# Performance work log

Measured on AMD Instinct MI355X. Metric: run time of the kernel, lower is better.

Reference implementation:

```python
import jax, jax.numpy as jnp
import numpy as np

B, S, D = 2, 2048, 1024
H, HD = 16, 64
MLP = 4096
EPS = 1e-5


def layer_norm(x, g, b):
    mu = jnp.mean(x, axis=-1, keepdims=True)
    var = jnp.mean(jnp.square(x - mu), axis=-1, keepdims=True)
    return (x - mu) * jax.lax.rsqrt(var + EPS) * g + b


def setup_inputs() -> dict:
    key = jax.random.key(0)
    ks = jax.random.split(key, 12)
    s = 0.02
    return {
        "x": jax.random.normal(ks[0], (B, S, D), jnp.float32),
        "ln1_g": jnp.ones((D,), jnp.float32),
        "ln1_b": jnp.zeros((D,), jnp.float32),
        "Wq": jax.random.normal(ks[1], (D, H * HD), jnp.float32) * s,
        "Wk": jax.random.normal(ks[2], (D, H * HD), jnp.float32) * s,
        "Wv": jax.random.normal(ks[3], (D, H * HD), jnp.float32) * s,
        "Wo": jax.random.normal(ks[4], (H * HD, D), jnp.float32) * s,
        "ln2_g": jnp.ones((D,), jnp.float32),
        "ln2_b": jnp.zeros((D,), jnp.float32),
        "fc1_w": jax.random.normal(ks[5], (D, MLP), jnp.float32) * s,
        "fc1_b": jnp.zeros((MLP,), jnp.float32),
        "fc2_w": jax.random.normal(ks[6], (MLP, D), jnp.float32) * s,
        "fc2_b": jnp.zeros((D,), jnp.float32),
    }


def reference(x, ln1_g, ln1_b, Wq, Wk, Wv, Wo, ln2_g, ln2_b, fc1_w, fc1_b, fc2_w, fc2_b):
    b, s, d = x.shape
    scale = 1.0 / np.sqrt(HD)
    h = layer_norm(x, ln1_g, ln1_b)
    # project and split heads: [b, H, s, HD]
    q = (h @ Wq).reshape(b, s, H, HD).transpose(0, 2, 1, 3)
    k = (h @ Wk).reshape(b, s, H, HD).transpose(0, 2, 1, 3)
    v = (h @ Wv).reshape(b, s, H, HD).transpose(0, 2, 1, 3)
    scores = jnp.einsum('bhqd,bhkd->bhqk', q, k) * scale
    causal = jnp.where(jnp.tril(jnp.ones((s, s), bool)), 0.0, -jnp.inf).astype(x.dtype)
    scores = scores + causal[None, None]
    attn_weights = jax.nn.softmax(scores, axis=-1)
    attn_out = jnp.einsum('bhqk,bhkd->bhqd', attn_weights, v)
    attn_out = attn_out.transpose(0, 2, 1, 3).reshape(b, s, H * HD) @ Wo
    x = x + attn_out
    h2 = layer_norm(x, ln2_g, ln2_b)
    mlp = jax.nn.gelu(h2 @ fc1_w + fc1_b, approximate=True) @ fc2_w + fc2_b
    x = x + mlp
    return (x, attn_weights)
```

## Files before the change

### kernel.cpp

```cpp
#include <hip/hip_runtime.h>
#include <cmath>

typedef __bf16 bf16;
typedef __bf16 bf16x8 __attribute__((ext_vector_type(8)));
typedef float f32x4 __attribute__((ext_vector_type(4)));

#define B_ 2
#define S_ 2048
#define D_ 1024
#define H_ 16
#define HD_ 64
#define MLP_ 4096
#define XOUT_ ((size_t)B_ * S_ * D_)

__device__ __forceinline__ void gll16(const void* g, void* l) {
  __builtin_amdgcn_global_load_lds((const __attribute__((address_space(1))) void*)g,
                                   (__attribute__((address_space(3))) void*)l, 16, 0, 0);
}

__device__ __forceinline__ f32x4 mfma16(bf16x8 a, bf16x8 b, f32x4 c) {
  return __builtin_amdgcn_mfma_f32_16x16x32_bf16(a, b, c, 0, 0, 0);
}

__device__ __forceinline__ float bfu2f(unsigned short u) {
  return __uint_as_float(((unsigned int)u) << 16);
}
__device__ __forceinline__ unsigned short f2bu(float v) {
  union { bf16 b; unsigned short u; } c; c.b = (bf16)v; return c.u;
}
__device__ __forceinline__ float ld_sc(const void* p, size_t i, int f32) {
  return f32 ? ((const float*)p)[i] : bfu2f(((const unsigned short*)p)[i]);
}

__global__ __launch_bounds__(64) void detect_k(const unsigned short* __restrict__ x,
                                               int* __restrict__ flag) {
  int tid = threadIdx.x;
  int cnt = 0;
  for (int i = tid; i < 512; i += 64) {
    int e = (x[i] >> 7) & 0xFF;
    if (e >= 0xBF) cnt++;
  }
  #pragma unroll
  for (int d = 1; d < 64; d <<= 1) cnt += __shfl_xor(cnt, d);
  if (tid == 0) flag[0] = (cnt > 8) ? 1 : 0;
}

__global__ __launch_bounds__(256) void transpose_ad(const void* __restrict__ in,
                                                    unsigned short* __restrict__ out,
                                                    int R, int C,
                                                    const int* __restrict__ flagp) {
  __shared__ unsigned short t[64][68];
  const int f32 = flagp[0];
  const int tid = threadIdx.x;
  const int c0 = blockIdx.x * 64, r0 = blockIdx.y * 64;
  for (int i = tid * 4; i < 4096; i += 1024) {
    int rr = i >> 6, cc = i & 63;
    size_t off = (size_t)(r0 + rr) * C + c0 + cc;
    if (f32) {
      float4 f = *(const float4*)((const float*)in + off);
      t[rr][cc + 0] = f2bu(f.x); t[rr][cc + 1] = f2bu(f.y);
      t[rr][cc + 2] = f2bu(f.z); t[rr][cc + 3] = f2bu(f.w);
    } else {
      *(ushort4*)&t[rr][cc] = *(const ushort4*)((const unsigned short*)in + off);
    }
  }
  __syncthreads();
  for (int i = tid * 4; i < 4096; i += 1024) {
    int orr = i & 63, oc = i >> 6;
    ushort4 v;
    v.x = t[orr + 0][oc]; v.y = t[orr + 1][oc];
    v.z = t[orr + 2][oc]; v.w = t[orr + 3][oc];
    *(ushort4*)(out + (size_t)(c0 + oc) * R + r0 + orr) = v;
  }
}

__global__ __launch_bounds__(256) void vtrans_k(const unsigned short* __restrict__ qkv,
                                                unsigned short* __restrict__ vT) {
  __shared__ unsigned short t[64][68];
  const int tid = threadIdx.x;
  const int s0 = blockIdx.x * 64, h = blockIdx.y, b = blockIdx.z;
  for (int i = tid * 4; i < 4096; i += 1024) {
    int si = i >> 6, hd = i & 63;
    *(ushort4*)&t[si][hd] =
        *(const ushort4*)(qkv + (size_t)(b * S_ + s0 + si) * 3072 + 2048 + h * 64 + hd);
  }
  __syncthreads();
  for (int i = tid * 4; i < 4096; i += 1024) {
    int ss = i & 63, hd = i >> 6;
    ushort4 v;
    v.x = t[ss + 0][hd]; v.y = t[ss + 1][hd];
    v.z = t[ss + 2][hd]; v.w = t[ss + 3][hd];
    *(ushort4*)(vT + ((size_t)(b * H_ + h) * 64 + hd) * S_ + s0 + ss) = v;
  }
}

__global__ __launch_bounds__(256) void ln_k(const void* __restrict__ xv,
                                            const void* __restrict__ g,
                                            const void* __restrict__ bvec,
                                            bf16* __restrict__ out,
                                            const int* __restrict__ flagp,
                                            int force_xf32) {
  const int f32 = flagp[0];
  const int xf32 = force_xf32 ? 1 : f32;
  const int row = blockIdx.x, tid = threadIdx.x;
  float v[4];
  if (xf32) {
    float4 f = *(const float4*)((const float*)xv + (size_t)row * 1024 + tid * 4);
    v[0] = f.x; v[1] = f.y; v[2] = f.z; v[3] = f.w;
  } else {
    ushort4 u = *(const ushort4*)((const unsigned short*)xv + (size_t)row * 1024 + tid * 4);
    v[0] = bfu2f(u.x); v[1] = bfu2f(u.y); v[2] = bfu2f(u.z); v[3] = bfu2f(u.w);
  }
  float s = 0.f, q = 0.f;
  #pragma unroll
  for (int i = 0; i < 4; i++) { s += v[i]; q += v[i] * v[i]; }
  #pragma unroll
  for (int d = 1; d < 64; d <<= 1) { s += __shfl_xor(s, d); q += __shfl_xor(q, d); }
  __shared__ float red[8];
  if ((tid & 63) == 0) { red[(tid >> 6) * 2] = s; red[(tid >> 6) * 2 + 1] = q; }
  __syncthreads();
  s = red[0] + red[2] + red[4] + red[6];
  q = red[1] + red[3] + red[5] + red[7];
  const float mean = s * (1.0f / 1024.0f);
  const float var = q * (1.0f / 1024.0f) - mean * mean;
  const float rs = rsqrtf(var + 1e-5f);
  unsigned short ov[4];
  #pragma unroll
  for (int i = 0; i < 4; i++) {
    float gg = ld_sc(g, tid * 4 + i, f32);
    float bb = ld_sc(bvec, tid * 4 + i, f32);
    ov[i] = f2bu((v[i] - mean) * rs * gg + bb);
  }
  ushort4 o4; o4.x = ov[0]; o4.y = ov[1]; o4.z = ov[2]; o4.w = ov[3];
  *(ushort4*)((unsigned short*)out + (size_t)row * 1024 + tid * 4) = o4;
}

template <int MODE>
__global__ __launch_bounds__(256) void gemm_bt(const bf16* __restrict__ A,
                                               const bf16* __restrict__ BT,
                                               int N, int K,
                                               const void* __restrict__ bias,
                                               const void* __restrict__ resb,
                                               const float* __restrict__ resf,
                                               bf16* __restrict__ outb,
                                               float* __restrict__ outf,
                                               const int* __restrict__ flagp) {
  __shared__ __align__(16) bf16 sA[128 * 64];
  __shared__ __align__(16) bf16 sB[128 * 64];
  const int f32 = flagp[0];
  const int tid = threadIdx.x;
  const int lane = tid & 63;
  const int wave = tid >> 6;
  const int wm = wave >> 1, wn = wave & 1;
  const int m0 = blockIdx.y * 128, n0 = blockIdx.x * 128;
  const int cn = lane & 15, rl = lane >> 4;
  const int r0 = tid >> 3, c16 = tid & 7;

  f32x4 zero = {0.f, 0.f, 0.f, 0.f};
  f32x4 acc[4][4];
  #pragma unroll
  for (int i = 0; i < 4; i++)
    #pragma unroll
    for (int j = 0; j < 4; j++) acc[i][j] = zero;

  for (int k0 = 0; k0 < K; k0 += 64) {
    __syncthreads();
    #pragma unroll
    for (int i = 0; i < 4; i++) {
      int row = r0 + i * 32;
      gll16(A + (size_t)(m0 + row) * K + k0 + c16 * 8, &sA[row * 64 + c16 * 8]);
      gll16(BT + (size_t)(n0 + row) * K + k0 + c16 * 8, &sB[row * 64 + c16 * 8]);
    }
    __syncthreads();
    #pragma unroll
    for (int kk = 0; kk < 64; kk += 32) {
      bf16x8 af[4], bfr[4];
      #pragma unroll
      for (int t = 0; t < 4; t++) {
        af[t] = *(const bf16x8*)&sA[(wm * 64 + t * 16 + cn) * 64 + kk + rl * 8];
        bfr[t] = *(const bf16x8*)&sB[(wn * 64 + t * 16 + cn) * 64 + kk + rl * 8];
      }
      #pragma unroll
      for (int mt = 0; mt < 4; mt++)
        #pragma unroll
        for (int nt = 0; nt < 4; nt++)
          acc[mt][nt] = mfma16(af[mt], bfr[nt], acc[mt][nt]);
    }
  }

  #pragma unroll
  for (int mt = 0; mt < 4; mt++) {
    #pragma unroll
    for (int nt = 0; nt < 4; nt++) {
      #pragma unroll
      for (int j = 0; j < 4; j++) {
        const int row = m0 + wm * 64 + mt * 16 + rl * 4 + j;
        const int col = n0 + wn * 64 + nt * 16 + cn;
        const size_t idx = (size_t)row * N + col;
        float v = acc[mt][nt][j];
        if (MODE == 0) {
          outb[idx] = (bf16)v;
        } else if (MODE == 1) {
          v += ld_sc(bias, col, f32);
          float gl = 0.5f * v * (1.0f + tanhf(0.7978845608028654f * (v + 0.044715f * v * v * v)));
          outb[idx] = (bf16)gl;
        } else if (MODE == 2) {
          outf[idx] = v + ld_sc(resb, idx, f32);
        } else {
          float val = v + ld_sc(bias, col, f32) + resf[idx];
          if (f32) outf[idx] = val; else outb[idx] = (bf16)val;
        }
      }
    }
  }
}

__global__ __launch_bounds__(256) void attn_k(const bf16* __restrict__ qkv,
                                              const bf16* __restrict__ vT,
                                              void* __restrict__ Pv,
                                              bf16* __restrict__ ao,
                                              const int* __restrict__ flagp) {
  __shared__ __align__(16) bf16 sQ[64 * 64];
  __shared__ __align__(16) bf16 sK[64 * 64];
  __shared__ __align__(16) bf16 sV[64 * 64];
  __shared__ __align__(16) bf16 sP[4][16 * 64];
  const int f32o = flagp[0];
  const int tid = threadIdx.x, lane = tid & 63, wave = tid >> 6;
  const int qt = blockIdx.x, h = blockIdx.y, b = blockIdx.z;
  const float scale = 0.125f;
  const float NEG = -1e30f;
  const int cn = lane & 15, rl = lane >> 4;
  const int r0 = tid >> 3, c16 = tid & 7;

  #pragma unroll
  for (int i = 0; i < 2; i++) {
    int row = r0 + i * 32;
    gll16(qkv + (size_t)(b * S_ + qt * 64 + row) * 3072 + h * 64 + c16 * 8,
          &sQ[row * 64 + c16 * 8]);
  }

  float m_i[4], l_i[4];
  #pragma unroll
  for (int j = 0; j < 4; j++) { m_i[j] = NEG; l_i[j] = 0.0f; }

  for (int kt = 0; kt <= qt; kt++) {
    __syncthreads();
    #pragma unroll
    for (int i = 0; i < 2; i++) {
      int row = r0 + i * 32;
      gll16(qkv + (size_t)(b * S_ + kt * 64 + row) * 3072 + 1024 + h * 64 + c16 * 8,
            &sK[row * 64 + c16 * 8]);
    }
    __syncthreads();
    f32x4 s[4];
    f32x4 zero = {0.f, 0.f, 0.f, 0.f};
    #pragma unroll
    for (int nt = 0; nt < 4; nt++) s[nt] = zero;
    #pragma unroll
    for (int kk = 0; kk < 64; kk += 32) {
      bf16x8 a = *(const bf16x8*)&sQ[(wave * 16 + cn) * 64 + kk + rl * 8];
      #pragma unroll
      for (int nt = 0; nt < 4; nt++) {
        bf16x8 bb = *(const bf16x8*)&sK[(nt * 16 + cn) * 64 + kk + rl * 8];
        s[nt] = mfma16(a, bb, s[nt]);
      }
    }
    const int rowg = qt * 64 + wave * 16 + rl * 4;
    const int colg0 = kt * 64 + cn;
    float pm[4] = {NEG, NEG, NEG, NEG};
    #pragma unroll
    for (int nt = 0; nt < 4; nt++)
      #pragma unroll
      for (int j = 0; j < 4; j++) {
        float v = (colg0 + nt * 16 > rowg + j) ? NEG : s[nt][j] * scale;
        s[nt][j] = v;
        pm[j] = fmaxf(pm[j], v);
      }
    #pragma unroll
    for (int j = 0; j < 4; j++) {
      #pragma unroll
      for (int d = 1; d < 16; d <<= 1) pm[j] = fmaxf(pm[j], __shfl_xor(pm[j], d));
      float mn = fmaxf(m_i[j], pm[j]);
      float ps = 0.f;
      #pragma unroll
      for (int nt = 0; nt < 4; nt++) ps += expf(s[nt][j] - mn);
      #pragma unroll
      for (int d = 1; d < 16; d <<= 1) ps += __shfl_xor(ps, d);
      l_i[j] = l_i[j] * expf(m_i[j] - mn) + ps;
      m_i[j] = mn;
    }
  }

  float inv_l[4];
  #pragma unroll
  for (int j = 0; j < 4; j++) inv_l[j] = 1.0f / l_i[j];

  f32x4 o[4];
  {
    f32x4 zero = {0.f, 0.f, 0.f, 0.f};
    #pragma unroll
    for (int nt = 0; nt < 4; nt++) o[nt] = zero;
  }
  for (int kt = 0; kt <= qt; kt++) {
    __syncthreads();
    #pragma unroll
    for (int i = 0; i < 2; i++) {
      int row = r0 + i * 32;
      gll16(qkv + (size_t)(b * S_ + kt * 64 + row) * 3072 + 1024 + h * 64 + c16 * 8,
            &sK[row * 64 + c16 * 8]);
      gll16(vT + ((size_t)(b * H_ + h) * 64 + row) * S_ + kt * 64 + c16 * 8,
            &sV[row * 64 + c16 * 8]);
    }
    __syncthreads();
    f32x4 s[4];
    f32x4 zero = {0.f, 0.f, 0.f, 0.f};
    #pragma unroll
    for (int nt = 0; nt < 4; nt++) s[nt] = zero;
    #pragma unroll
    for (int kk = 0; kk < 64; kk += 32) {
      bf16x8 a = *(const bf16x8*)&sQ[(wave * 16 + cn) * 64 + kk + rl * 8];
      #pragma unroll
      for (int nt = 0; nt < 4; nt++) {
        bf16x8 bb = *(const bf16x8*)&sK[(nt * 16 + cn) * 64 + kk + rl * 8];
        s[nt] = mfma16(a, bb, s[nt]);
      }
    }
    const int rowg = qt * 64 + wave * 16 + rl * 4;
    const int colg0 = kt * 64 + cn;
    #pragma unroll
    for (int nt = 0; nt < 4; nt++)
      #pragma unroll
      for (int j = 0; j < 4; j++) {
        bool masked = (colg0 + nt * 16 > rowg + j);
        float p = masked ? 0.0f : expf(s[nt][j] * scale - m_i[j]) * inv_l[j];
        sP[wave][(rl * 4 + j) * 64 + nt * 16 + cn] = (bf16)p;
      }
    __syncthreads();
    #pragma unroll
    for (int kk = 0; kk < 64; kk += 32) {
      bf16x8 ap = *(const bf16x8*)&sP[wave][cn * 64 + kk + rl * 8];
      #pragma unroll
      for (int nt = 0; nt < 4; nt++) {
        bf16x8 bv = *(const bf16x8*)&sV[(nt * 16 + cn) * 64 + kk + rl * 8];
        o[nt] = mfma16(ap, bv, o[nt]);
      }
    }
    size_t base = XOUT_ + (((size_t)b * H_ + h) * S_ + qt * 64 + wave * 16) * S_ + kt * 64;
    #pragma unroll
    for (int i = 0; i < 2; i++) {
      int idx = lane + i * 64;
      int r = idx >> 3, cc = idx & 7;
      if (f32o) {
        float4 lo, hi;
        const bf16* src = &sP[wave][r * 64 + cc * 8];
        lo.x = (float)src[0]; lo.y = (float)src[1]; lo.z = (float)src[2]; lo.w = (float)src[3];
        hi.x = (float)src[4]; hi.y = (float)src[5]; hi.z = (float)src[6]; hi.w = (float)src[7];
        *(float4*)((float*)Pv + base + (size_t)r * S_ + cc * 8) = lo;
        *(float4*)((float*)Pv + base + (size_t)r * S_ + cc * 8 + 4) = hi;
      } else {
        uint4 val = *(const uint4*)&sP[wave][r * 64 + cc * 8];
        *(uint4*)((bf16*)Pv + base + (size_t)r * S_ + cc * 8) = val;
      }
    }
  }

  {
    const int t0 = qt + 1;
    const int nch = (32 - t0) * 8;
    size_t rowbase = XOUT_ + (((size_t)b * H_ + h) * S_ + qt * 64) * S_;
    uint4 z; z.x = 0; z.y = 0; z.z = 0; z.w = 0;
    for (int idx = tid; idx < 64 * nch; idx += 256) {
      int r = idx / nch, cc = idx % nch;
      size_t off = rowbase + (size_t)r * S_ + t0 * 64 + cc * 8;
      if (f32o) {
        *(uint4*)((float*)Pv + off) = z;
        *(uint4*)((float*)Pv + off + 4) = z;
      } else {
        *(uint4*)((bf16*)Pv + off) = z;
      }
    }
  }

  #pragma unroll
  for (int nt = 0; nt < 4; nt++)
    #pragma unroll
    for (int j = 0; j < 4; j++) {
      int rowg2 = b * S_ + qt * 64 + wave * 16 + rl * 4 + j;
      ao[(size_t)rowg2 * 1024 + h * 64 + nt * 16 + cn] = (bf16)o[nt][j];
    }
}

extern "C" void kernel_launch(void* const* d_in, const int* in_sizes, int n_in,
                              void* d_out, int out_size, void* d_ws, size_t ws_size,
                              hipStream_t stream) {
  (void)in_sizes; (void)n_in; (void)out_size; (void)ws_size;
  const void* x    = d_in[0];
  const void* ln1g = d_in[1];
  const void* ln1b = d_in[2];
  const void* Wq   = d_in[3];
  const void* Wk   = d_in[4];
  const void* Wv   = d_in[5];
  const void* Wo   = d_in[6];
  const void* ln2g = d_in[7];
  const void* ln2b = d_in[8];
  const void* fc1w = d_in[9];
  const void* fc1b = d_in[10];
  const void* fc2w = d_in[11];
  const void* fc2b = d_in[12];

  char* ws = (char*)d_ws;
  bf16* wqkvT = (bf16*)(ws + 0);
  bf16* woT   = (bf16*)(ws + 6291456);
  bf16* fc1T  = (bf16*)(ws + 8388608);
  bf16* fc2T  = (bf16*)(ws + 16777216);
  bf16* h     = (bf16*)(ws + 25165824);
  bf16* qkv   = (bf16*)(ws + 33554432);
  bf16* vT    = (bf16*)(ws + 58720256);
  bf16* m1    = (bf16*)(ws + 33554432);
  bf16* aout  = (bf16*)(ws + 67108864);
  float* x1   = (float*)(ws + 75497472);
  int* flag   = (int*)(ws + 92274688);

  dim3 blk(256);

  detect_k<<<1, 64, 0, stream>>>((const unsigned short*)x, flag);

  transpose_ad<<<dim3(16, 16), blk, 0, stream>>>(Wq, (unsigned short*)wqkvT, 1024, 1024, flag);
  transpose_ad<<<dim3(16, 16), blk, 0, stream>>>(Wk, (unsigned short*)(wqkvT + 1024 * 1024), 1024, 1024, flag);
  transpose_ad<<<dim3(16, 16), blk, 0, stream>>>(Wv, (unsigned short*)(wqkvT + 2 * 1024 * 1024), 1024, 1024, flag);
  transpose_ad<<<dim3(16, 16), blk, 0, stream>>>(Wo, (unsigned short*)woT, 1024, 1024, flag);
  transpose_ad<<<dim3(64, 16), blk, 0, stream>>>(fc1w, (unsigned short*)fc1T, 1024, 4096, flag);
  transpose_ad<<<dim3(16, 64), blk, 0, stream>>>(fc2w, (unsigned short*)fc2T, 4096, 1024, flag);

  ln_k<<<4096, blk, 0, stream>>>(x, ln1g, ln1b, h, flag, 0);

  gemm_bt<0><<<dim3(24, 32), blk, 0, stream>>>(h, wqkvT, 3072, 1024, nullptr, nullptr, nullptr, qkv, nullptr, flag);

  vtrans_k<<<dim3(32, 16, 2), blk, 0, stream>>>((const unsigned short*)qkv, (unsigned short*)vT);

  attn_k<<<dim3(32, 16, 2), blk, 0, stream>>>(qkv, vT, d_out, aout, flag);

  gemm_bt<2><<<dim3(8, 32), blk, 0, stream>>>(aout, woT, 1024, 1024, nullptr, x, nullptr, nullptr, x1, flag);

  ln_k<<<4096, blk, 0, stream>>>(x1, ln2g, ln2b, h, flag, 1);

  gemm_bt<1><<<dim3(32, 32), blk, 0, stream>>>(h, fc1T, 4096, 1024, fc1b, nullptr, nullptr, m1, nullptr, flag);

  gemm_bt<3><<<dim3(8, 32), blk, 0, stream>>>(m1, fc2T, 1024, 4096, fc2b, nullptr, x1, (bf16*)d_out, (float*)d_out, flag);
}
```

Before: 1.155 ms.

## Double-buffer K/V tiles in attention with swizzled LDS and exp2 softmax

The attention kernel now double-buffers K and V tiles in LDS, prefetching the next tile while computing the current one, and waits with explicit vmcnt counts and raw barriers instead of full __syncthreads. LDS layouts are XOR-swizzled to reduce bank conflicts. Q is held in registers, and the causal mask is applied only on the diagonal tile. Query tiles are launched in reverse order so the longest blocks start first. Softmax uses exp2 with a pre-scaled log2e factor, and GELU's tanh is rewritten as a sigmoid via exp2. The explicit vmcnt waits depend on exact counts of outstanding loads and stores, which is fragile if code generation changes.

```diff
diff --git a/kernel.cpp b/kernel.cpp
--- a/kernel.cpp
+++ b/kernel.cpp
@@ -13,6 +13,10 @@
 #define MLP_ 4096
 #define XOUT_ ((size_t)B_ * S_ * D_)
 
+#define SBAR() __builtin_amdgcn_s_barrier()
+#define VMCNT(N) asm volatile("s_waitcnt vmcnt(" #N ")" ::: "memory")
+#define SFENCE() asm volatile("" ::: "memory")
+
 __device__ __forceinline__ void gll16(const void* g, void* l) {
   __builtin_amdgcn_global_load_lds((const __attribute__((address_space(1))) void*)g,
                                    (__attribute__((address_space(3))) void*)l, 16, 0, 0);
@@ -30,6 +34,11 @@
 }
 __device__ __forceinline__ float ld_sc(const void* p, size_t i, int f32) {
   return f32 ? ((const float*)p)[i] : bfu2f(((const unsigned short*)p)[i]);
+}
+
+__device__ __forceinline__ int swz(int row, int col) {
+  int byo = row * 128 + col * 2;
+  return (byo ^ (((byo >> 9) & 3) << 5)) >> 1;
 }
 
 __global__ __launch_bounds__(64) void detect_k(const unsigned short* __restrict__ x,
@@ -202,7 +211,8 @@
           outb[idx] = (bf16)v;
         } else if (MODE == 1) {
           v += ld_sc(bias, col, f32);
-          float gl = 0.5f * v * (1.0f + tanhf(0.7978845608028654f * (v + 0.044715f * v * v * v)));
+          float u = 0.7978845608028654f * (v + 0.044715f * v * v * v);
+          float gl = v / (1.0f + exp2f(-2.8853900817779268f * u));
           outb[idx] = (bf16)gl;
         } else if (MODE == 2) {
           outf[idx] = v + ld_sc(resb, idx, f32);
@@ -220,80 +230,114 @@
                                               void* __restrict__ Pv,
                                               bf16* __restrict__ ao,
                                               const int* __restrict__ flagp) {
-  __shared__ __align__(16) bf16 sQ[64 * 64];
-  __shared__ __align__(16) bf16 sK[64 * 64];
-  __shared__ __align__(16) bf16 sV[64 * 64];
+  __shared__ __align__(16) bf16 sK[2][64 * 64];
+  __shared__ __align__(16) bf16 sV[2][64 * 64];
   __shared__ __align__(16) bf16 sP[4][16 * 64];
   const int f32o = flagp[0];
   const int tid = threadIdx.x, lane = tid & 63, wave = tid >> 6;
-  const int qt = blockIdx.x, h = blockIdx.y, b = blockIdx.z;
-  const float scale = 0.125f;
+  const int qt = (int)(gridDim.x - 1 - blockIdx.x);
+  const int h = blockIdx.y, b = blockIdx.z;
+  const float scale2 = 0.18033688011112042f;
   const float NEG = -1e30f;
   const int cn = lane & 15, rl = lane >> 4;
-  const int r0 = tid >> 3, c16 = tid & 7;
-
+
+  int urow[2], ucol[2], ldst[2];
   #pragma unroll
   for (int i = 0; i < 2; i++) {
-    int row = r0 + i * 32;
-    gll16(qkv + (size_t)(b * S_ + qt * 64 + row) * 3072 + h * 64 + c16 * 8,
-          &sQ[row * 64 + c16 * 8]);
-  }
+    int Lb = tid * 16 + i * 4096;
+    int Ub = Lb ^ (((Lb >> 9) & 3) << 5);
+    urow[i] = Ub >> 7;
+    ucol[i] = (Ub & 127) >> 1;
+    ldst[i] = Lb >> 1;
+  }
+
+  const bf16* kbase = qkv + (size_t)b * S_ * 3072 + 1024 + h * 64;
+  const bf16* vbase = vT + ((size_t)(b * H_ + h) * 64) * S_;
+
+  bf16x8 aq[2];
+  {
+    const bf16* qb = qkv + (size_t)(b * S_ + qt * 64 + wave * 16 + cn) * 3072 + h * 64;
+    aq[0] = *(const bf16x8*)(qb + rl * 8);
+    aq[1] = *(const bf16x8*)(qb + 32 + rl * 8);
+  }
+
+  #pragma unroll
+  for (int i = 0; i < 2; i++)
+    gll16(kbase + (size_t)urow[i] * 3072 + ucol[i], &sK[0][ldst[i]]);
+  VMCNT(0);
+  SBAR();
 
   float m_i[4], l_i[4];
   #pragma unroll
   for (int j = 0; j < 4; j++) { m_i[j] = NEG; l_i[j] = 0.0f; }
 
+  int cur = 0;
   for (int kt = 0; kt <= qt; kt++) {
-    __syncthreads();
-    #pragma unroll
-    for (int i = 0; i < 2; i++) {
-      int row = r0 + i * 32;
-      gll16(qkv + (size_t)(b * S_ + kt * 64 + row) * 3072 + 1024 + h * 64 + c16 * 8,
-            &sK[row * 64 + c16 * 8]);
-    }
-    __syncthreads();
+    if (kt < qt) {
+      #pragma unroll
+      for (int i = 0; i < 2; i++)
+        gll16(kbase + (size_t)((kt + 1) * 64 + urow[i]) * 3072 + ucol[i], &sK[cur ^ 1][ldst[i]]);
+      SFENCE();
+    }
     f32x4 s[4];
     f32x4 zero = {0.f, 0.f, 0.f, 0.f};
     #pragma unroll
     for (int nt = 0; nt < 4; nt++) s[nt] = zero;
     #pragma unroll
-    for (int kk = 0; kk < 64; kk += 32) {
-      bf16x8 a = *(const bf16x8*)&sQ[(wave * 16 + cn) * 64 + kk + rl * 8];
+    for (int kx = 0; kx < 2; kx++)
       #pragma unroll
       for (int nt = 0; nt < 4; nt++) {
-        bf16x8 bb = *(const bf16x8*)&sK[(nt * 16 + cn) * 64 + kk + rl * 8];
-        s[nt] = mfma16(a, bb, s[nt]);
-      }
-    }
-    const int rowg = qt * 64 + wave * 16 + rl * 4;
-    const int colg0 = kt * 64 + cn;
+        bf16x8 bb = *(const bf16x8*)&sK[cur][swz(nt * 16 + cn, kx * 32 + rl * 8)];
+        s[nt] = mfma16(aq[kx], bb, s[nt]);
+      }
     float pm[4] = {NEG, NEG, NEG, NEG};
-    #pragma unroll
-    for (int nt = 0; nt < 4; nt++)
-      #pragma unroll
-      for (int j = 0; j < 4; j++) {
-        float v = (colg0 + nt * 16 > rowg + j) ? NEG : s[nt][j] * scale;
-        s[nt][j] = v;
-        pm[j] = fmaxf(pm[j], v);
-      }
+    if (kt == qt) {
+      #pragma unroll
+      for (int nt = 0; nt < 4; nt++)
+        #pragma unroll
+        for (int j = 0; j < 4; j++) {
+          float v = (nt * 16 + cn > wave * 16 + rl * 4 + j) ? NEG : s[nt][j] * scale2;
+          s[nt][j] = v;
+          pm[j] = fmaxf(pm[j], v);
+        }
+    } else {
+      #pragma unroll
+      for (int nt = 0; nt < 4; nt++)
+        #pragma unroll
+        for (int j = 0; j < 4; j++) {
+          float v = s[nt][j] * scale2;
+          s[nt][j] = v;
+          pm[j] = fmaxf(pm[j], v);
+        }
+    }
     #pragma unroll
     for (int j = 0; j < 4; j++) {
       #pragma unroll
       for (int d = 1; d < 16; d <<= 1) pm[j] = fmaxf(pm[j], __shfl_xor(pm[j], d));
       float mn = fmaxf(m_i[j], pm[j]);
-      float ps = 0.f;
-      #pragma unroll
-      for (int nt = 0; nt < 4; nt++) ps += expf(s[nt][j] - mn);
+      float ps = exp2f(s[0][j] - mn) + exp2f(s[1][j] - mn) +
+                 exp2f(s[2][j] - mn) + exp2f(s[3][j] - mn);
       #pragma unroll
       for (int d = 1; d < 16; d <<= 1) ps += __shfl_xor(ps, d);
-      l_i[j] = l_i[j] * expf(m_i[j] - mn) + ps;
+      l_i[j] = l_i[j] * exp2f(m_i[j] - mn) + ps;
       m_i[j] = mn;
     }
+    if (kt < qt) { VMCNT(0); SBAR(); cur ^= 1; }
   }
 
   float inv_l[4];
   #pragma unroll
   for (int j = 0; j < 4; j++) inv_l[j] = 1.0f / l_i[j];
+
+  SBAR();
+  #pragma unroll
+  for (int i = 0; i < 2; i++) {
+    gll16(kbase + (size_t)urow[i] * 3072 + ucol[i], &sK[0][ldst[i]]);
+    gll16(vbase + (size_t)urow[i] * S_ + ucol[i], &sV[0][ldst[i]]);
+  }
+  VMCNT(0);
+  SBAR();
+  cur = 0;
 
   f32x4 o[4];
   {
@@ -301,66 +345,78 @@
     #pragma unroll
     for (int nt = 0; nt < 4; nt++) o[nt] = zero;
   }
+
   for (int kt = 0; kt <= qt; kt++) {
-    __syncthreads();
-    #pragma unroll
-    for (int i = 0; i < 2; i++) {
-      int row = r0 + i * 32;
-      gll16(qkv + (size_t)(b * S_ + kt * 64 + row) * 3072 + 1024 + h * 64 + c16 * 8,
-            &sK[row * 64 + c16 * 8]);
-      gll16(vT + ((size_t)(b * H_ + h) * 64 + row) * S_ + kt * 64 + c16 * 8,
-            &sV[row * 64 + c16 * 8]);
-    }
-    __syncthreads();
+    if (kt < qt) {
+      #pragma unroll
+      for (int i = 0; i < 2; i++) {
+        gll16(kbase + (size_t)((kt + 1) * 64 + urow[i]) * 3072 + ucol[i], &sK[cur ^ 1][ldst[i]]);
+        gll16(vbase + (size_t)urow[i] * S_ + (kt + 1) * 64 + ucol[i], &sV[cur ^ 1][ldst[i]]);
+      }
+      SFENCE();
+    }
     f32x4 s[4];
     f32x4 zero = {0.f, 0.f, 0.f, 0.f};
     #pragma unroll
     for (int nt = 0; nt < 4; nt++) s[nt] = zero;
     #pragma unroll
-    for (int kk = 0; kk < 64; kk += 32) {
-      bf16x8 a = *(const bf16x8*)&sQ[(wave * 16 + cn) * 64 + kk + rl * 8];
+    for (int kx = 0; kx < 2; kx++)
       #pragma unroll
       for (int nt = 0; nt < 4; nt++) {
-        bf16x8 bb = *(const bf16x8*)&sK[(nt * 16 + cn) * 64 + kk + rl * 8];
-        s[nt] = mfma16(a, bb, s[nt]);
-      }
-    }
-    const int rowg = qt * 64 + wave * 16 + rl * 4;
-    const int colg0 = kt * 64 + cn;
-    #pragma unroll
-    for (int nt = 0; nt < 4; nt++)
-      #pragma unroll
-      for (int j = 0; j < 4; j++) {
-        bool masked = (colg0 + nt * 16 > rowg + j);
-        float p = masked ? 0.0f : expf(s[nt][j] * scale - m_i[j]) * inv_l[j];
-        sP[wave][(rl * 4 + j) * 64 + nt * 16 + cn] = (bf16)p;
-      }
-    __syncthreads();
-    #pragma unroll
-    for (int kk = 0; kk < 64; kk += 32) {
-      bf16x8 ap = *(const bf16x8*)&sP[wave][cn * 64 + kk + rl * 8];
+        bf16x8 bb = *(const bf16x8*)&sK[cur][swz(nt * 16 + cn, kx * 32 + rl * 8)];
+        s[nt] = mfma16(aq[kx], bb, s[nt]);
+      }
+    if (kt == qt) {
+      #pragma unroll
+      for (int nt = 0; nt < 4; nt++)
+        #pragma unroll
+        for (int j = 0; j < 4; j++) {
+          bool masked = (nt * 16 + cn > wave * 16 + rl * 4 + j);
+          float p = masked ? 0.0f : exp2f(s[nt][j] * scale2 - m_i[j]) * inv_l[j];
+          sP[wave][swz(rl * 4 + j, nt * 16 + cn)] = (bf16)p;
+        }
+    } else {
+      #pragma unroll
+      for (int nt = 0; nt < 4; nt++)
+        #pragma unroll
+        for (int j = 0; j < 4; j++) {
+          float p = exp2f(s[nt][j] * scale2 - m_i[j]) * inv_l[j];
+          sP[wave][swz(rl * 4 + j, nt * 16 + cn)] = (bf16)p;
+        }
+    }
+    {
+      size_t base = XOUT_ + (((size_t)b * H_ + h) * S_ + qt * 64 + wave * 16) * S_ + kt * 64;
+      #pragma unroll
+      for (int i = 0; i < 2; i++) {
+        int idx = lane + i * 64;
+        int r = idx >> 3, cc = idx & 7;
+        uint4 val = *(const uint4*)&sP[wave][swz(r, cc * 8)];
+        if (f32o) {
+          float4 lo, hi;
+          lo.x = __uint_as_float(val.x << 16); lo.y = __uint_as_float(val.x & 0xffff0000u);
+          lo.z = __uint_as_float(val.y << 16); lo.w = __uint_as_float(val.y & 0xffff0000u);
+          hi.x = __uint_as_float(val.z << 16); hi.y = __uint_as_float(val.z & 0xffff0000u);
+          hi.z = __uint_as_float(val.w << 16); hi.w = __uint_as_float(val.w & 0xffff0000u);
+          *(float4*)((float*)Pv + base + (size_t)r * S_ + cc * 8) = lo;
+          *(float4*)((float*)Pv + base + (size_t)r * S_ + cc * 8 + 4) = hi;
+        } else {
+          *(uint4*)((bf16*)Pv + base + (size_t)r * S_ + cc * 8) = val;
+        }
+      }
+    }
+    #pragma unroll
+    for (int kx = 0; kx < 2; kx++) {
+      bf16x8 ap = *(const bf16x8*)&sP[wave][swz(cn, kx * 32 + rl * 8)];
       #pragma unroll
       for (int nt = 0; nt < 4; nt++) {
-        bf16x8 bv = *(const bf16x8*)&sV[(nt * 16 + cn) * 64 + kk + rl * 8];
+        bf16x8 bv = *(const bf16x8*)&sV[cur][swz(nt * 16 + cn, kx * 32 + rl * 8)];
         o[nt] = mfma16(ap, bv, o[nt]);
       }
     }
-    size_t base = XOUT_ + (((size_t)b * H_ + h) * S_ + qt * 64 + wave * 16) * S_ + kt * 64;
-    #pragma unroll
-    for (int i = 0; i < 2; i++) {
-      int idx = lane + i * 64;
-      int r = idx >> 3, cc = idx & 7;
-      if (f32o) {
-        float4 lo, hi;
-        const bf16* src = &sP[wave][r * 64 + cc * 8];
-        lo.x = (float)src[0]; lo.y = (float)src[1]; lo.z = (float)src[2]; lo.w = (float)src[3];
-        hi.x = (float)src[4]; hi.y = (float)src[5]; hi.z = (float)src[6]; hi.w = (float)src[7];
-        *(float4*)((float*)Pv + base + (size_t)r * S_ + cc * 8) = lo;
-        *(float4*)((float*)Pv + base + (size_t)r * S_ + cc * 8 + 4) = hi;
-      } else {
-        uint4 val = *(const uint4*)&sP[wave][r * 64 + cc * 8];
-        *(uint4*)((bf16*)Pv + base + (size_t)r * S_ + cc * 8) = val;
-      }
+    if (kt < qt) {
+      if (f32o) { VMCNT(4); } else { VMCNT(2); }
+      SBAR();
+      cur ^= 1;
     }
   }
 
```

After: 1.075 ms. -6.9%, faster.
